# Kernel optimization log

Measured on AMD Instinct MI355X. Metric: run time of the kernel, lower is better.

The kernel has to match this reference:

```python
import jax, jax.numpy as jnp
import numpy as np

L, B, T, C, H, FC = 8, 4, 2048, 1024, 16, 4
HD = C // H  # head dim = 64
DFF = FC * C  # 4096


def _layernorm(x, g, b, eps=1e-5):
    mu = jnp.mean(x, axis=-1, keepdims=True)
    var = jnp.mean(jnp.square(x - mu), axis=-1, keepdims=True)
    return (x - mu) * jax.lax.rsqrt(var + eps) * g + b


def setup_inputs() -> dict:
    key = jax.random.key(0)
    ks = jax.random.split(key, 18)
    s = 0.02
    d = {}
    d["x"] = jax.random.normal(ks[0], (B, T, C), jnp.float32)
    d["ln1_g"] = jnp.ones((L, C), jnp.float32)
    d["ln1_b"] = jnp.zeros((L, C), jnp.float32)
    d["ln2_g"] = jnp.ones((L, C), jnp.float32)
    d["ln2_b"] = jnp.zeros((L, C), jnp.float32)
    d["wq"] = jax.random.normal(ks[1], (L, C, C), jnp.float32) * s
    d["bq"] = jnp.zeros((L, C), jnp.float32)
    d["wk"] = jax.random.normal(ks[2], (L, C, C), jnp.float32) * s
    d["bk"] = jnp.zeros((L, C), jnp.float32)
    d["wv"] = jax.random.normal(ks[3], (L, C, C), jnp.float32) * s
    d["bv"] = jnp.zeros((L, C), jnp.float32)
    d["wo"] = jax.random.normal(ks[4], (L, C, C), jnp.float32) * s
    d["bo"] = jnp.zeros((L, C), jnp.float32)
    d["w1"] = jax.random.normal(ks[5], (L, C, DFF), jnp.float32) * s
    d["b1"] = jnp.zeros((L, DFF), jnp.float32)
    d["w2"] = jax.random.normal(ks[6], (L, DFF, C), jnp.float32) * s
    d["b2"] = jnp.zeros((L, C), jnp.float32)
    return d


def _forward(x, ln1_g, ln1_b, ln2_g, ln2_b, wq, bq, wk, bk, wv, bv, wo, bo, w1, b1, w2, b2):
    mask = jnp.tril(jnp.ones((T, T), dtype=bool))  # causal mask (block_size buffer)
    scale = 1.0 / np.sqrt(HD).astype(np.float32)

    def block(h, p):
        g1, be1, g2, be2, Wq, Bq, Wk, Bk, Wv, Bv, Wo, Bo, W1, B1, W2, B2 = p
        hn = _layernorm(h, g1, be1)
        # heads: [B, H, T, HD]
        q = (hn @ Wq + Bq).reshape(B, T, H, HD).transpose(0, 2, 1, 3)
        k = (hn @ Wk + Bk).reshape(B, T, H, HD).transpose(0, 2, 1, 3)
        v = (hn @ Wv + Bv).reshape(B, T, H, HD).transpose(0, 2, 1, 3)
        att = jnp.einsum('bhid,bhjd->bhij', q, k) * scale
        att = jnp.where(mask, att, -jnp.inf)
        att = jax.nn.softmax(att, axis=-1)
        y = jnp.einsum('bhij,bhjd->bhid', att, v)
        y = y.transpose(0, 2, 1, 3).reshape(B, T, C) @ Wo + Bo
        h = h + y
        m = _layernorm(h, g2, be2)
        h = h + jax.nn.gelu(m @ W1 + B1, approximate=False) @ W2 + B2
        return h, None

    params = (ln1_g, ln1_b, ln2_g, ln2_b, wq, bq, wk, bk, wv, bv, wo, bo, w1, b1, w2, b2)
    x, _ = jax.lax.scan(block, x, params)
    return x


def reference(x, ln1_g, ln1_b, ln2_g, ln2_b, wq, bq, wk, bk, wv, bv, wo, bo, w1, b1, w2, b2):
    return _forward(x, ln1_g, ln1_b, ln2_g, ln2_b, wq, bq, wk, bk, wv, bv, wo, bo, w1, b1, w2, b2)
```

## Files before the change

### kernel.cpp

```cpp
#include <hip/hip_runtime.h>
#include <hip/hip_bf16.h>

#define LL 8
#define BBx 4
#define TT 2048
#define CC 1024
#define HH 16
#define HDD 64
#define DFFx 4096
#define MMx 8192

typedef __bf16 bf16;
typedef __attribute__((ext_vector_type(8))) __bf16 bf16x8;
typedef __attribute__((ext_vector_type(4))) __bf16 bf16x4;
typedef __attribute__((ext_vector_type(4))) float f32x4;
typedef __attribute__((ext_vector_type(8))) unsigned short u16x8;

__device__ __forceinline__ unsigned short bfbits(float v) {
  return __builtin_bit_cast(unsigned short, (__bf16)v);
}

__device__ __forceinline__ int xcd_swz(int id, int nwg) {
  return (id & 7) * (nwg >> 3) + (id >> 3);
}

#define GLDS(gp, lp) __builtin_amdgcn_global_load_lds( \
    (const __attribute__((address_space(1))) void*)(gp), \
    (__attribute__((address_space(3))) void*)(lp), 16, 0, 0)

__global__ __launch_bounds__(256) void transpose_cast(
    const float* __restrict__ W, bf16* __restrict__ Wt,
    int K, int N, long srcStride, long dstStride)
{
  __shared__ float tile[32][33];
  const float* Wl = W + (size_t)blockIdx.z * srcStride;
  bf16* Wtl = Wt + (size_t)blockIdx.z * dstStride;
  const int n0 = blockIdx.x * 32, k0 = blockIdx.y * 32;
  const int tx = threadIdx.x, ty = threadIdx.y;
#pragma unroll
  for (int i = 0; i < 32; i += 8)
    tile[ty + i][tx] = Wl[(size_t)(k0 + ty + i) * N + n0 + tx];
  __syncthreads();
#pragma unroll
  for (int i = 0; i < 32; i += 8)
    Wtl[(size_t)(n0 + ty + i) * K + k0 + tx] = (bf16)tile[tx][ty + i];
}

__global__ __launch_bounds__(256) void ln_cmb(
    float* __restrict__ h, const float* __restrict__ p0, const float* __restrict__ p1,
    const float* __restrict__ gamma, const float* __restrict__ beta,
    bf16* __restrict__ out)
{
  const int row = blockIdx.x, tid = threadIdx.x;
  const size_t base = (size_t)row * CC + tid * 4;
  float4 v = *(const float4*)(h + base);
  if (p0) {
    const float4 a = *(const float4*)(p0 + base);
    const float4 b = *(const float4*)(p1 + base);
    v.x += a.x + b.x; v.y += a.y + b.y; v.z += a.z + b.z; v.w += a.w + b.w;
    *(float4*)(h + base) = v;
  }
  if (!out) return;
  float s  = v.x + v.y + v.z + v.w;
  float ss = v.x * v.x + v.y * v.y + v.z * v.z + v.w * v.w;
#pragma unroll
  for (int o = 32; o >= 1; o >>= 1) {
    s  += __shfl_xor(s, o);
    ss += __shfl_xor(ss, o);
  }
  __shared__ float rs[4], rss[4];
  const int w = tid >> 6, l = tid & 63;
  if (l == 0) { rs[w] = s; rss[w] = ss; }
  __syncthreads();
  s  = rs[0] + rs[1] + rs[2] + rs[3];
  ss = rss[0] + rss[1] + rss[2] + rss[3];
  const float mu = s * (1.f / CC);
  const float rstd = rsqrtf(ss * (1.f / CC) - mu * mu + 1e-5f);
  const float4 g  = *(const float4*)(gamma + tid * 4);
  const float4 be = *(const float4*)(beta + tid * 4);
  bf16x4 o4;
  o4[0] = (bf16)((v.x - mu) * rstd * g.x + be.x);
  o4[1] = (bf16)((v.y - mu) * rstd * g.y + be.y);
  o4[2] = (bf16)((v.z - mu) * rstd * g.z + be.z);
  o4[3] = (bf16)((v.w - mu) * rstd * g.w + be.w);
  *(bf16x4*)(out + (size_t)row * CC + tid * 4) = o4;
}

template<int EPI>
__global__ __launch_bounds__(256, 4) void gemm128(
    const bf16* __restrict__ A, const bf16* __restrict__ Bt,
    const float* __restrict__ bias0, const float* __restrict__ bias1,
    const float* __restrict__ bias2,
    bf16* __restrict__ o0, bf16* __restrict__ o1, bf16* __restrict__ o2,
    float* __restrict__ p0, float* __restrict__ p1,
    int M, int N, int K, int lda)
{
  __shared__ __align__(16) bf16 sA[128 * 64];
  __shared__ __align__(16) bf16 sB[128 * 64];
  const int nx = N >> 7;
  int wk = xcd_swz((int)blockIdx.x, (int)gridDim.x);
  int koff = 0;
  float* part = p0;
  bool addb = true;
  if constexpr (EPI == 1) {
    const int tiles = nx * (M >> 7);
    const int ks = wk / tiles;
    wk -= ks * tiles;
    koff = ks * K;
    addb = (ks == 0);
    part = ks ? p1 : p0;
  }
  const int m0 = (wk / nx) * 128;
  const int n0 = (wk % nx) * 128;
  const int tid = threadIdx.x;
  const int w = tid >> 6, l = tid & 63;
  const int wr = w >> 1, wc = w & 1;
  const int lr = l & 15, lk = l >> 4;

  f32x4 acc[4][4] = {};
  const int NT = K >> 6;

  for (int kt = 0; kt < NT; ++kt) {
#pragma unroll
    for (int i = 0; i < 4; ++i) {
      const int e = (tid << 4) + (i << 12);
      const int ro = e >> 7, co = (e & 127) >> 1;
      GLDS(A + (size_t)(m0 + ro) * lda + kt * 64 + koff + co, sA + (e >> 1));
      GLDS(Bt + (size_t)(n0 + ro) * lda + kt * 64 + koff + co, sB + (e >> 1));
    }
    __syncthreads();
#pragma unroll
    for (int kk = 0; kk < 2; ++kk) {
      bf16x8 af[4], bfr[4];
#pragma unroll
      for (int i = 0; i < 4; ++i)
        af[i] = *(const bf16x8*)&sA[(wr * 64 + i * 16 + lr) * 64 + kk * 32 + lk * 8];
#pragma unroll
      for (int j = 0; j < 4; ++j)
        bfr[j] = *(const bf16x8*)&sB[(wc * 64 + j * 16 + lr) * 64 + kk * 32 + lk * 8];
#pragma unroll
      for (int i = 0; i < 4; ++i)
#pragma unroll
        for (int j = 0; j < 4; ++j)
          acc[i][j] = __builtin_amdgcn_mfma_f32_16x16x32_bf16(af[i], bfr[j], acc[i][j], 0, 0, 0);
    }
    __syncthreads();
  }

  if constexpr (EPI == 0) {
    const int seg = n0 >> 10;
    const float* bp = (seg == 0) ? bias0 : (seg == 1 ? bias1 : bias2);
    if (seg < 2) {
      float bv4[4];
#pragma unroll
      for (int j = 0; j < 4; ++j) bv4[j] = bp[(n0 + wc * 64 + j * 16 + lr) & 1023];
      const int hh = ((n0 + wc * 64) & 1023) >> 6;
      bf16* dst = (seg == 0) ? o0 : o1;
#pragma unroll
      for (int i = 0; i < 4; ++i) {
        const int mrow = m0 + wr * 64 + i * 16 + lk * 4;
        const int bidx = mrow >> 11, t = mrow & 2047;
#pragma unroll
        for (int r = 0; r < 4; ++r) {
          bf16* rowp = dst + (((size_t)(bidx * HH + hh)) * TT + t + r) * HDD;
#pragma unroll
          for (int j = 0; j < 4; ++j)
            rowp[j * 16 + lr] = (bf16)(acc[i][j][r] + bv4[j]);
        }
      }
    } else {
      char* scb = (w < 2) ? ((char*)sA + w * 8192) : ((char*)sB + (w - 2) * 8192);
#pragma unroll
      for (int j = 0; j < 4; ++j) {
        const int dl = j * 16 + lr;
        const float bv = bias2[(n0 + wc * 64 + dl) & 1023];
#pragma unroll
        for (int i = 0; i < 4; ++i) {
          ushort4 pk;
          pk.x = bfbits(acc[i][j][0] + bv);
          pk.y = bfbits(acc[i][j][1] + bv);
          pk.z = bfbits(acc[i][j][2] + bv);
          pk.w = bfbits(acc[i][j][3] + bv);
          *(ushort4*)(scb + dl * 128 + (((i * 16 + lk * 4) * 2) ^ ((dl & 7) << 4))) = pk;
        }
      }
      asm volatile("s_waitcnt lgkmcnt(0)" ::: "memory");
      const int hh = ((n0 + wc * 64) & 1023) >> 6;
      const int bidx = (m0 + wr * 64) >> 11;
      const int tb = (m0 + wr * 64) & 2047;
      const int c = l & 7;
#pragma unroll
      for (int g = 0; g < 8; ++g) {
        const int dl = g * 8 + (l >> 3);
        u16x8 val = *(const u16x8*)(scb + dl * 128 + ((c * 16) ^ ((dl & 7) << 4)));
        *(u16x8*)&o2[(((size_t)(bidx * HH + hh)) * HDD + dl) * TT + tb + c * 8] = val;
      }
    }
  } else if constexpr (EPI == 1) {
    float bv4[4];
#pragma unroll
    for (int j = 0; j < 4; ++j)
      bv4[j] = addb ? bias0[n0 + wc * 64 + j * 16 + lr] : 0.f;
#pragma unroll
    for (int i = 0; i < 4; ++i) {
      const int mrow = m0 + wr * 64 + i * 16 + lk * 4;
#pragma unroll
      for (int r = 0; r < 4; ++r) {
        float* rowp = part + (size_t)(mrow + r) * N + n0 + wc * 64;
#pragma unroll
        for (int j = 0; j < 4; ++j)
          rowp[j * 16 + lr] = acc[i][j][r] + bv4[j];
      }
    }
  } else {
    float bv4[4];
#pragma unroll
    for (int j = 0; j < 4; ++j) bv4[j] = bias0[n0 + wc * 64 + j * 16 + lr];
#pragma unroll
    for (int i = 0; i < 4; ++i) {
      const int mrow = m0 + wr * 64 + i * 16 + lk * 4;
#pragma unroll
      for (int r = 0; r < 4; ++r) {
        bf16* rowp = o0 + (size_t)(mrow + r) * N + n0 + wc * 64;
#pragma unroll
        for (int j = 0; j < 4; ++j) {
          const float x = acc[i][j][r] + bv4[j];
          rowp[j * 16 + lr] = (bf16)(0.5f * x * (1.f + erff(x * 0.70710678f)));
        }
      }
    }
  }
  (void)M;
}

__global__ __launch_bounds__(256) void attn_fwd(
    const bf16* __restrict__ Q, const bf16* __restrict__ Kk,
    const bf16* __restrict__ Vt, bf16* __restrict__ O)
{
  const int wk = xcd_swz((int)blockIdx.x, (int)gridDim.x);
  const int bh = wk >> 3;
  const int xt = wk & 7;
  const int tid = threadIdx.x;
  const int w = tid >> 6, l = tid & 63;
  const int lr = l & 15, lk = l >> 4;
  const int bidx = bh >> 4, hh = bh & 15;

  const bf16* Qp = Q  + (size_t)bh * (TT * HDD);
  const bf16* Kp = Kk + (size_t)bh * (TT * HDD);
  const bf16* Vp = Vt + (size_t)bh * (HDD * TT);

  __shared__ __align__(16) bf16 sK[64 * 64];
  __shared__ __align__(16) bf16 sV[64 * 64];
  __shared__ __align__(16) bf16 sP[4][16 * 64];
  bf16* sPw = &sP[w][0];

  const float sc = 0.125f;
  const int swz = (lr & 7) * 8;
  const int srow = tid >> 3;
  const int scol = (((tid & 7) ^ (srow & 7)) << 3);
  const int sdst = tid << 3;

  for (int half = 0; half < 2; ++half) {
    const int qtile = (half == 0) ? xt : (15 - xt);
    const int q0 = qtile * 128;

    bf16x8 qf[2][2];
#pragma unroll
    for (int qi = 0; qi < 2; ++qi)
#pragma unroll
      for (int dk = 0; dk < 2; ++dk)
        qf[qi][dk] = *(const bf16x8*)&Qp[(size_t)(q0 + w * 32 + qi * 16 + lr) * HDD + dk * 32 + lk * 8];

    f32x4 accO[2][4] = {};
    float mrun[2] = {-__builtin_inff(), -__builtin_inff()};
    float lrun[2] = {0.f, 0.f};
    const int wqmax = q0 + w * 32 + 31;
    const int kvend = q0 + 128;

    for (int kv = 0; kv < kvend; kv += 64) {
      __syncthreads();
#pragma unroll
      for (int i = 0; i < 2; ++i) {
        GLDS(Kp + (size_t)(kv + srow + i * 32) * HDD + scol, sK + sdst + i * 2048);
        GLDS(Vp + (size_t)(srow + i * 32) * TT + kv + scol, sV + sdst + i * 2048);
      }
      __syncthreads();

      if (kv <= wqmax) {
#pragma unroll
        for (int qi = 0; qi < 2; ++qi) {
          f32x4 st[4];
#pragma unroll
          for (int kt = 0; kt < 4; ++kt) {
            f32x4 z = {0.f, 0.f, 0.f, 0.f};
#pragma unroll
            for (int dk = 0; dk < 2; ++dk) {
              bf16x8 kf = *(const bf16x8*)&sK[(kt * 16 + lr) * 64 + ((dk * 32 + lk * 8) ^ swz)];
              z = __builtin_amdgcn_mfma_f32_16x16x32_bf16(kf, qf[qi][dk], z, 0, 0, 0);
            }
            st[kt] = z;
          }
          const int qabs = q0 + w * 32 + qi * 16 + lr;
          float pm = -__builtin_inff();
#pragma unroll
          for (int kt = 0; kt < 4; ++kt)
#pragma unroll
            for (int r = 0; r < 4; ++r) {
              const int kvabs = kv + kt * 16 + lk * 4 + r;
              float val = st[kt][r] * sc;
              val = (kvabs > qabs) ? -__builtin_inff() : val;
              st[kt][r] = val;
              pm = fmaxf(pm, val);
            }
          pm = fmaxf(pm, __shfl_xor(pm, 16));
          pm = fmaxf(pm, __shfl_xor(pm, 32));
          const float mnew = fmaxf(mrun[qi], pm);
          const float alpha = __expf(mrun[qi] - mnew);
          mrun[qi] = mnew;
          float psum = 0.f;
#pragma unroll
          for (int kt = 0; kt < 4; ++kt) {
            const float p0v = __expf(st[kt][0] - mnew);
            const float p1v = __expf(st[kt][1] - mnew);
            const float p2v = __expf(st[kt][2] - mnew);
            const float p3v = __expf(st[kt][3] - mnew);
            psum += p0v + p1v + p2v + p3v;
            ushort4 pk;
            pk.x = bfbits(p0v); pk.y = bfbits(p1v); pk.z = bfbits(p2v); pk.w = bfbits(p3v);
            *(ushort4*)&sPw[lr * 64 + ((kt * 16 + lk * 4) ^ swz)] = pk;
          }
          psum += __shfl_xor(psum, 16);
          psum += __shfl_xor(psum, 32);
          lrun[qi] = lrun[qi] * alpha + psum;
          f32x4 al4;
#pragma unroll
          for (int r = 0; r < 4; ++r) al4[r] = __shfl(alpha, lk * 4 + r);
#pragma unroll
          for (int dj = 0; dj < 4; ++dj) accO[qi][dj] *= al4;
#pragma unroll
          for (int kt2 = 0; kt2 < 2; ++kt2) {
            bf16x8 pf = *(const bf16x8*)&sPw[lr * 64 + ((kt2 * 32 + lk * 8) ^ swz)];
#pragma unroll
            for (int dj = 0; dj < 4; ++dj) {
              bf16x8 vf = *(const bf16x8*)&sV[(dj * 16 + lr) * 64 + ((kt2 * 32 + lk * 8) ^ swz)];
              accO[qi][dj] = __builtin_amdgcn_mfma_f32_16x16x32_bf16(pf, vf, accO[qi][dj], 0, 0, 0);
            }
          }
        }
      }
    }

#pragma unroll
    for (int qi = 0; qi < 2; ++qi) {
      const float linv = 1.f / lrun[qi];
      f32x4 li4;
#pragma unroll
      for (int r = 0; r < 4; ++r) li4[r] = __shfl(linv, lk * 4 + r);
      const int tbase = q0 + w * 32 + qi * 16 + lk * 4;
#pragma unroll
      for (int dj = 0; dj < 4; ++dj)
#pragma unroll
        for (int r = 0; r < 4; ++r)
          O[((size_t)bidx * TT + tbase + r) * CC + hh * 64 + dj * 16 + lr] =
              (bf16)(accO[qi][dj][r] * li4[r]);
    }
  }
}

extern "C" void kernel_launch(void* const* d_in, const int* in_sizes, int n_in,
                              void* d_out, int out_size, void* d_ws, size_t ws_size,
                              hipStream_t stream)
{
  const float* x    = (const float*)d_in[0];
  const float* ln1g = (const float*)d_in[1];
  const float* ln1b = (const float*)d_in[2];
  const float* ln2g = (const float*)d_in[3];
  const float* ln2b = (const float*)d_in[4];
  const float* wq   = (const float*)d_in[5];
  const float* bq   = (const float*)d_in[6];
  const float* wk   = (const float*)d_in[7];
  const float* bk   = (const float*)d_in[8];
  const float* wv   = (const float*)d_in[9];
  const float* bvv  = (const float*)d_in[10];
  const float* wo   = (const float*)d_in[11];
  const float* bo   = (const float*)d_in[12];
  const float* w1   = (const float*)d_in[13];
  const float* b1   = (const float*)d_in[14];
  const float* w2   = (const float*)d_in[15];
  const float* b2   = (const float*)d_in[16];

  float* h = (float*)d_out;
  bf16* ws = (bf16*)d_ws;
  bf16* wqkvT = ws;
  bf16* woT   = wqkvT + (size_t)LL * 3 * CC * CC;
  bf16* w1T   = woT + (size_t)LL * CC * CC;
  bf16* w2T   = w1T + (size_t)LL * CC * DFFx;
  bf16* hn    = w2T + (size_t)LL * CC * DFFx;
  bf16* qb    = hn + (size_t)MMx * CC;
  bf16* kb    = qb + (size_t)MMx * CC;
  bf16* vt    = kb + (size_t)MMx * CC;
  bf16* ab    = vt + (size_t)MMx * CC;
  bf16* mid   = ab + (size_t)MMx * CC;

  float* pw0 = (float*)mid;
  float* pw1 = (float*)mid + (size_t)MMx * CC;
  float* pm0 = (float*)qb;
  float* pm1 = (float*)vt;

  hipMemcpyAsync(h, x, (size_t)MMx * CC * sizeof(float), hipMemcpyDeviceToDevice, stream);

  dim3 tb(32, 8);
  transpose_cast<<<dim3(CC / 32, CC / 32, LL), tb, 0, stream>>>(wq, wqkvT, CC, CC, (long)CC * CC, (long)3 * CC * CC);
  transpose_cast<<<dim3(CC / 32, CC / 32, LL), tb, 0, stream>>>(wk, wqkvT + CC * CC, CC, CC, (long)CC * CC, (long)3 * CC * CC);
  transpose_cast<<<dim3(CC / 32, CC / 32, LL), tb, 0, stream>>>(wv, wqkvT + 2 * CC * CC, CC, CC, (long)CC * CC, (long)3 * CC * CC);
  transpose_cast<<<dim3(CC / 32, CC / 32, LL), tb, 0, stream>>>(wo, woT, CC, CC, (long)CC * CC, (long)CC * CC);
  transpose_cast<<<dim3(DFFx / 32, CC / 32, LL), tb, 0, stream>>>(w1, w1T, CC, DFFx, (long)CC * DFFx, (long)CC * DFFx);
  transpose_cast<<<dim3(CC / 32, DFFx / 32, LL), tb, 0, stream>>>(w2, w2T, DFFx, CC, (long)CC * DFFx, (long)CC * DFFx);

  for (int li = 0; li < LL; ++li) {
    if (li == 0)
      ln_cmb<<<MMx, 256, 0, stream>>>(h, nullptr, nullptr, ln1g, ln1b, hn);
    else
      ln_cmb<<<MMx, 256, 0, stream>>>(h, pm0, pm1, ln1g + li * CC, ln1b + li * CC, hn);
    gemm128<0><<<(3 * CC / 128) * (MMx / 128), 256, 0, stream>>>(
        hn, wqkvT + (size_t)li * 3 * CC * CC, bq + li * CC, bk + li * CC, bvv + li * CC,
        qb, kb, vt, nullptr, nullptr, MMx, 3 * CC, CC, CC);
    attn_fwd<<<8 * BBx * HH, 256, 0, stream>>>(qb, kb, vt, ab);
    gemm128<1><<<2 * (CC / 128) * (MMx / 128), 256, 0, stream>>>(
        ab, woT + (size_t)li * CC * CC, bo + li * CC, nullptr, nullptr,
        nullptr, nullptr, nullptr, pw0, pw1, MMx, CC, CC / 2, CC);
    ln_cmb<<<MMx, 256, 0, stream>>>(h, pw0, pw1, ln2g + li * CC, ln2b + li * CC, hn);
    gemm128<2><<<(DFFx / 128) * (MMx / 128), 256, 0, stream>>>(
        hn, w1T + (size_t)li * CC * DFFx, b1 + li * DFFx, nullptr, nullptr,
        mid, nullptr, nullptr, nullptr, nullptr, MMx, DFFx, CC, CC);
    gemm128<1><<<2 * (CC / 128) * (MMx / 128), 256, 0, stream>>>(
        mid, w2T + (size_t)li * CC * DFFx, b2 + li * CC, nullptr, nullptr,
        nullptr, nullptr, nullptr, pm0, pm1, MMx, CC, DFFx / 2, DFFx);
  }
  ln_cmb<<<MMx, 256, 0, stream>>>(h, pm0, pm1, nullptr, nullptr, nullptr);
  (void)in_sizes; (void)n_in; (void)out_size; (void)ws_size;
}
```

Measured before the change: 3.320 ms.

## Double-buffer K/V tiles in attention with async prefetch and MFMA priority

Converts the attention kernel's K/V shared-memory staging to double buffering: the next 64-key tile is issued via direct global-to-LDS loads before computing on the current one. Explicit vmcnt waits and raw barriers replace the two __syncthreads per iteration. It also raises wave priority around the MFMA sections. This doubles K/V LDS usage, which may reduce occupancy, and relies on the vmcnt(4) count matching the number of outstanding loads.

Result: no change. 3.360 ms (+1.2%).

```diff
diff --git a/kernel.cpp b/kernel.cpp
--- a/kernel.cpp
+++ b/kernel.cpp
@@ -249,8 +249,8 @@
   const bf16* Kp = Kk + (size_t)bh * (TT * HDD);
   const bf16* Vp = Vt + (size_t)bh * (HDD * TT);
 
-  __shared__ __align__(16) bf16 sK[64 * 64];
-  __shared__ __align__(16) bf16 sV[64 * 64];
+  __shared__ __align__(16) bf16 sK[2][64 * 64];
+  __shared__ __align__(16) bf16 sV[2][64 * 64];
   __shared__ __align__(16) bf16 sP[4][16 * 64];
   bf16* sPw = &sP[w][0];
 
@@ -260,6 +260,14 @@
   const int scol = (((tid & 7) ^ (srow & 7)) << 3);
   const int sdst = tid << 3;
 
+  auto stageKV = [&](int b, int kv) {
+#pragma unroll
+    for (int i = 0; i < 2; ++i) {
+      GLDS(Kp + (size_t)(kv + srow + i * 32) * HDD + scol, &sK[b][sdst + i * 2048]);
+      GLDS(Vp + (size_t)(srow + i * 32) * TT + kv + scol, &sV[b][sdst + i * 2048]);
+    }
+  };
+
   for (int half = 0; half < 2; ++half) {
     const int qtile = (half == 0) ? xt : (15 - xt);
     const int q0 = qtile * 128;
@@ -270,6 +278,7 @@
 #pragma unroll
       for (int dk = 0; dk < 2; ++dk)
         qf[qi][dk] = *(const bf16x8*)&Qp[(size_t)(q0 + w * 32 + qi * 16 + lr) * HDD + dk * 32 + lk * 8];
+    __builtin_amdgcn_sched_barrier(0);
 
     f32x4 accO[2][4] = {};
     float mrun[2] = {-__builtin_inff(), -__builtin_inff()};
@@ -277,29 +286,35 @@
     const int wqmax = q0 + w * 32 + 31;
     const int kvend = q0 + 128;
 
+    stageKV(0, 0);
+    int cur = 0;
     for (int kv = 0; kv < kvend; kv += 64) {
-      __syncthreads();
-#pragma unroll
-      for (int i = 0; i < 2; ++i) {
-        GLDS(Kp + (size_t)(kv + srow + i * 32) * HDD + scol, sK + sdst + i * 2048);
-        GLDS(Vp + (size_t)(srow + i * 32) * TT + kv + scol, sV + sdst + i * 2048);
-      }
-      __syncthreads();
+      if (kv + 64 < kvend) {
+        stageKV(cur ^ 1, kv + 64);
+        asm volatile("s_waitcnt vmcnt(4)" ::: "memory");
+      } else {
+        asm volatile("s_waitcnt vmcnt(0)" ::: "memory");
+      }
+      __builtin_amdgcn_s_barrier();
+      const bf16* sKc = &sK[cur][0];
+      const bf16* sVc = &sV[cur][0];
 
       if (kv <= wqmax) {
 #pragma unroll
         for (int qi = 0; qi < 2; ++qi) {
           f32x4 st[4];
+          __builtin_amdgcn_s_setprio(1);
 #pragma unroll
           for (int kt = 0; kt < 4; ++kt) {
             f32x4 z = {0.f, 0.f, 0.f, 0.f};
 #pragma unroll
             for (int dk = 0; dk < 2; ++dk) {
-              bf16x8 kf = *(const bf16x8*)&sK[(kt * 16 + lr) * 64 + ((dk * 32 + lk * 8) ^ swz)];
+              bf16x8 kf = *(const bf16x8*)&sKc[(kt * 16 + lr) * 64 + ((dk * 32 + lk * 8) ^ swz)];
               z = __builtin_amdgcn_mfma_f32_16x16x32_bf16(kf, qf[qi][dk], z, 0, 0, 0);
             }
             st[kt] = z;
           }
+          __builtin_amdgcn_s_setprio(0);
           const int qabs = q0 + w * 32 + qi * 16 + lr;
           float pm = -__builtin_inff();
 #pragma unroll
@@ -337,17 +352,21 @@
           for (int r = 0; r < 4; ++r) al4[r] = __shfl(alpha, lk * 4 + r);
 #pragma unroll
           for (int dj = 0; dj < 4; ++dj) accO[qi][dj] *= al4;
+          __builtin_amdgcn_s_setprio(1);
 #pragma unroll
           for (int kt2 = 0; kt2 < 2; ++kt2) {
             bf16x8 pf = *(const bf16x8*)&sPw[lr * 64 + ((kt2 * 32 + lk * 8) ^ swz)];
 #pragma unroll
             for (int dj = 0; dj < 4; ++dj) {
-              bf16x8 vf = *(const bf16x8*)&sV[(dj * 16 + lr) * 64 + ((kt2 * 32 + lk * 8) ^ swz)];
+              bf16x8 vf = *(const bf16x8*)&sVc[(dj * 16 + lr) * 64 + ((kt2 * 32 + lk * 8) ^ swz)];
               accO[qi][dj] = __builtin_amdgcn_mfma_f32_16x16x32_bf16(pf, vf, accO[qi][dj], 0, 0, 0);
             }
           }
+          __builtin_amdgcn_s_setprio(0);
         }
       }
+      __builtin_amdgcn_s_barrier();
+      cur ^= 1;
     }
 
 #pragma unroll
```

## Fuse residual add into GEMM epilogue, drop split-K, fold softmax scale into Q

Applied to the files above, without the earlier changes.

The projection and FC2 GEMMs no longer use split-K into two partial buffers. They now add their result in place to the fp32 residual, so the residual-combine pass in the layernorm kernel and the final combine kernel go away. Q is pre-scaled by log2(e)/sqrt(d) in the QKV epilogue so attention can use exp2 and skip the per-element scale. The causal mask is applied only on diagonal tiles. Without split-K the N=1024 GEMMs launch half as many workgroups (512), which may underfill the GPU, and the FC2 GEMM now runs a longer K loop per tile.

New measurement: 3.585 ms. +8.0%, slower.

```diff
diff --git a/kernel.cpp b/kernel.cpp
--- a/kernel.cpp
+++ b/kernel.cpp
@@ -15,6 +15,8 @@
 typedef __attribute__((ext_vector_type(4))) __bf16 bf16x4;
 typedef __attribute__((ext_vector_type(4))) float f32x4;
 typedef __attribute__((ext_vector_type(8))) unsigned short u16x8;
+
+#define QSCALE 0.18033688f
 
 __device__ __forceinline__ unsigned short bfbits(float v) {
   return __builtin_bit_cast(unsigned short, (__bf16)v);
@@ -46,21 +48,12 @@
     Wtl[(size_t)(n0 + ty + i) * K + k0 + tx] = (bf16)tile[tx][ty + i];
 }
 
-__global__ __launch_bounds__(256) void ln_cmb(
-    float* __restrict__ h, const float* __restrict__ p0, const float* __restrict__ p1,
-    const float* __restrict__ gamma, const float* __restrict__ beta,
-    bf16* __restrict__ out)
+__global__ __launch_bounds__(256) void ln_fwd(
+    const float* __restrict__ h, const float* __restrict__ gamma,
+    const float* __restrict__ beta, bf16* __restrict__ out)
 {
   const int row = blockIdx.x, tid = threadIdx.x;
-  const size_t base = (size_t)row * CC + tid * 4;
-  float4 v = *(const float4*)(h + base);
-  if (p0) {
-    const float4 a = *(const float4*)(p0 + base);
-    const float4 b = *(const float4*)(p1 + base);
-    v.x += a.x + b.x; v.y += a.y + b.y; v.z += a.z + b.z; v.w += a.w + b.w;
-    *(float4*)(h + base) = v;
-  }
-  if (!out) return;
+  const float4 v = *(const float4*)(h + (size_t)row * CC + tid * 4);
   float s  = v.x + v.y + v.z + v.w;
   float ss = v.x * v.x + v.y * v.y + v.z * v.z + v.w * v.w;
 #pragma unroll
@@ -92,24 +85,12 @@
     const float* __restrict__ bias0, const float* __restrict__ bias1,
     const float* __restrict__ bias2,
     bf16* __restrict__ o0, bf16* __restrict__ o1, bf16* __restrict__ o2,
-    float* __restrict__ p0, float* __restrict__ p1,
-    int M, int N, int K, int lda)
+    float* __restrict__ resid, int M, int N, int K)
 {
   __shared__ __align__(16) bf16 sA[128 * 64];
   __shared__ __align__(16) bf16 sB[128 * 64];
   const int nx = N >> 7;
-  int wk = xcd_swz((int)blockIdx.x, (int)gridDim.x);
-  int koff = 0;
-  float* part = p0;
-  bool addb = true;
-  if constexpr (EPI == 1) {
-    const int tiles = nx * (M >> 7);
-    const int ks = wk / tiles;
-    wk -= ks * tiles;
-    koff = ks * K;
-    addb = (ks == 0);
-    part = ks ? p1 : p0;
-  }
+  const int wk = xcd_swz((int)blockIdx.x, (int)gridDim.x);
   const int m0 = (wk / nx) * 128;
   const int n0 = (wk % nx) * 128;
   const int tid = threadIdx.x;
@@ -125,8 +106,8 @@
     for (int i = 0; i < 4; ++i) {
       const int e = (tid << 4) + (i << 12);
       const int ro = e >> 7, co = (e & 127) >> 1;
-      GLDS(A + (size_t)(m0 + ro) * lda + kt * 64 + koff + co, sA + (e >> 1));
-      GLDS(Bt + (size_t)(n0 + ro) * lda + kt * 64 + koff + co, sB + (e >> 1));
+      GLDS(A + (size_t)(m0 + ro) * K + kt * 64 + co, sA + (e >> 1));
+      GLDS(Bt + (size_t)(n0 + ro) * K + kt * 64 + co, sB + (e >> 1));
     }
     __syncthreads();
 #pragma unroll
@@ -151,6 +132,7 @@
     const int seg = n0 >> 10;
     const float* bp = (seg == 0) ? bias0 : (seg == 1 ? bias1 : bias2);
     if (seg < 2) {
+      const float qs = (seg == 0) ? QSCALE : 1.0f;
       float bv4[4];
 #pragma unroll
       for (int j = 0; j < 4; ++j) bv4[j] = bp[(n0 + wc * 64 + j * 16 + lr) & 1023];
@@ -165,7 +147,7 @@
           bf16* rowp = dst + (((size_t)(bidx * HH + hh)) * TT + t + r) * HDD;
 #pragma unroll
           for (int j = 0; j < 4; ++j)
-            rowp[j * 16 + lr] = (bf16)(acc[i][j][r] + bv4[j]);
+            rowp[j * 16 + lr] = (bf16)((acc[i][j][r] + bv4[j]) * qs);
         }
       }
     } else {
@@ -199,17 +181,16 @@
   } else if constexpr (EPI == 1) {
     float bv4[4];
 #pragma unroll
-    for (int j = 0; j < 4; ++j)
-      bv4[j] = addb ? bias0[n0 + wc * 64 + j * 16 + lr] : 0.f;
+    for (int j = 0; j < 4; ++j) bv4[j] = bias0[n0 + wc * 64 + j * 16 + lr];
 #pragma unroll
     for (int i = 0; i < 4; ++i) {
       const int mrow = m0 + wr * 64 + i * 16 + lk * 4;
 #pragma unroll
       for (int r = 0; r < 4; ++r) {
-        float* rowp = part + (size_t)(mrow + r) * N + n0 + wc * 64;
+        float* rowp = resid + (size_t)(mrow + r) * N + n0 + wc * 64;
 #pragma unroll
         for (int j = 0; j < 4; ++j)
-          rowp[j * 16 + lr] = acc[i][j][r] + bv4[j];
+          rowp[j * 16 + lr] += acc[i][j][r] + bv4[j];
       }
     }
   } else {
@@ -254,7 +235,6 @@
   __shared__ __align__(16) bf16 sP[4][16 * 64];
   bf16* sPw = &sP[w][0];
 
-  const float sc = 0.125f;
   const int swz = (lr & 7) * 8;
   const int srow = tid >> 3;
   const int scol = (((tid & 7) ^ (srow & 7)) << 3);
@@ -300,30 +280,37 @@
             }
             st[kt] = z;
           }
-          const int qabs = q0 + w * 32 + qi * 16 + lr;
+          const int qabs_base = q0 + w * 32 + qi * 16;
           float pm = -__builtin_inff();
-#pragma unroll
-          for (int kt = 0; kt < 4; ++kt)
-#pragma unroll
-            for (int r = 0; r < 4; ++r) {
-              const int kvabs = kv + kt * 16 + lk * 4 + r;
-              float val = st[kt][r] * sc;
-              val = (kvabs > qabs) ? -__builtin_inff() : val;
-              st[kt][r] = val;
-              pm = fmaxf(pm, val);
-            }
+          if (kv + 63 > qabs_base) {
+            const int qabs = qabs_base + lr;
+#pragma unroll
+            for (int kt = 0; kt < 4; ++kt)
+#pragma unroll
+              for (int r = 0; r < 4; ++r) {
+                const int kvabs = kv + kt * 16 + lk * 4 + r;
+                float val = (kvabs > qabs) ? -__builtin_inff() : st[kt][r];
+                st[kt][r] = val;
+                pm = fmaxf(pm, val);
+              }
+          } else {
+#pragma unroll
+            for (int kt = 0; kt < 4; ++kt)
+#pragma unroll
+              for (int r = 0; r < 4; ++r) pm = fmaxf(pm, st[kt][r]);
+          }
           pm = fmaxf(pm, __shfl_xor(pm, 16));
           pm = fmaxf(pm, __shfl_xor(pm, 32));
           const float mnew = fmaxf(mrun[qi], pm);
-          const float alpha = __expf(mrun[qi] - mnew);
+          const float alpha = exp2f(mrun[qi] - mnew);
           mrun[qi] = mnew;
           float psum = 0.f;
 #pragma unroll
           for (int kt = 0; kt < 4; ++kt) {
-            const float p0v = __expf(st[kt][0] - mnew);
-            const float p1v = __expf(st[kt][1] - mnew);
-            const float p2v = __expf(st[kt][2] - mnew);
-            const float p3v = __expf(st[kt][3] - mnew);
+            const float p0v = exp2f(st[kt][0] - mnew);
+            const float p1v = exp2f(st[kt][1] - mnew);
+            const float p2v = exp2f(st[kt][2] - mnew);
+            const float p3v = exp2f(st[kt][3] - mnew);
             psum += p0v + p1v + p2v + p3v;
             ushort4 pk;
             pk.x = bfbits(p0v); pk.y = bfbits(p1v); pk.z = bfbits(p2v); pk.w = bfbits(p3v);
@@ -402,11 +389,6 @@
   bf16* ab    = vt + (size_t)MMx * CC;
   bf16* mid   = ab + (size_t)MMx * CC;
 
-  float* pw0 = (float*)mid;
-  float* pw1 = (float*)mid + (size_t)MMx * CC;
-  float* pm0 = (float*)qb;
-  float* pm1 = (float*)vt;
-
   hipMemcpyAsync(h, x, (size_t)MMx * CC * sizeof(float), hipMemcpyDeviceToDevice, stream);
 
   dim3 tb(32, 8);
@@ -418,25 +400,21 @@
   transpose_cast<<<dim3(CC / 32, DFFx / 32, LL), tb, 0, stream>>>(w2, w2T, DFFx, CC, (long)CC * DFFx, (long)CC * DFFx);
 
   for (int li = 0; li < LL; ++li) {
-    if (li == 0)
-      ln_cmb<<<MMx, 256, 0, stream>>>(h, nullptr, nullptr, ln1g, ln1b, hn);
-    else
-      ln_cmb<<<MMx, 256, 0, stream>>>(h, pm0, pm1, ln1g + li * CC, ln1b + li * CC, hn);
+    ln_fwd<<<MMx, 256, 0, stream>>>(h, ln1g + li * CC, ln1b + li * CC, hn);
     gemm128<0><<<(3 * CC / 128) * (MMx / 128), 256, 0, stream>>>(
         hn, wqkvT + (size_t)li * 3 * CC * CC, bq + li * CC, bk + li * CC, bvv + li * CC,
-        qb, kb, vt, nullptr, nullptr, MMx, 3 * CC, CC, CC);
+        qb, kb, vt, nullptr, MMx, 3 * CC, CC);
     attn_fwd<<<8 * BBx * HH, 256, 0, stream>>>(qb, kb, vt, ab);
-    gemm128<1><<<2 * (CC / 128) * (MMx / 128), 256, 0, stream>>>(
+    gemm128<1><<<(CC / 128) * (MMx / 128), 256, 0, stream>>>(
         ab, woT + (size_t)li * CC * CC, bo + li * CC, nullptr, nullptr,
-        nullptr, nullptr, nullptr, pw0, pw1, MMx, CC, CC / 2, CC);
-    ln_cmb<<<MMx, 256, 0, stream>>>(h, pw0, pw1, ln2g + li * CC, ln2b + li * CC, hn);
+        nullptr, nullptr, nullptr, h, MMx, CC, CC);
+    ln_fwd<<<MMx, 256, 0, stream>>>(h, ln2g + li * CC, ln2b + li * CC, hn);
     gemm128<2><<<(DFFx / 128) * (MMx / 128), 256, 0, stream>>>(
         hn, w1T + (size_t)li * CC * DFFx, b1 + li * DFFx, nullptr, nullptr,
-        mid, nullptr, nullptr, nullptr, nullptr, MMx, DFFx, CC, CC);
-    gemm128<1><<<2 * (CC / 128) * (MMx / 128), 256, 0, stream>>>(
+        mid, nullptr, nullptr, nullptr, MMx, DFFx, CC);
+    gemm128<1><<<(CC / 128) * (MMx / 128), 256, 0, stream>>>(
         mid, w2T + (size_t)li * CC * DFFx, b2 + li * CC, nullptr, nullptr,
-        nullptr, nullptr, nullptr, pm0, pm1, MMx, CC, DFFx / 2, DFFx);
+        nullptr, nullptr, nullptr, h, MMx, CC, DFFx);
   }
-  ln_cmb<<<MMx, 256, 0, stream>>>(h, pm0, pm1, nullptr, nullptr, nullptr);
   (void)in_sizes; (void)n_in; (void)out_size; (void)ws_size;
 }
```
